# Kernel tuning notes

Hardware: AMD Instinct MI355X
Metric: run time of the kernel (lower is better)

Reference implementation:

```python
import jax, jax.numpy as jnp
import numpy as np

S, B, SC = 2048, 1024, 256 * 16  # shops, bundles, styles*colors


def setup_inputs() -> dict:
    key = jax.random.key(0)
    k1, k2, k3, k4 = jax.random.split(key, 4)
    return {
        "proba": jax.random.normal(k1, (S * B,), dtype=jnp.float32),
        "cur_inven": jax.random.uniform(k2, (S, SC), dtype=jnp.float32),
        "bun_sc": jax.random.uniform(k3, (B, SC), dtype=jnp.float32),
        "avail_bundle": jax.random.uniform(k4, (B,), dtype=jnp.float32),
        "alloc_bundle": jnp.zeros((B,), dtype=jnp.float32),
    }


def reference(proba, cur_inven, bun_sc, avail_bundle, alloc_bundle):
    # proba[i] with i = shop*B + bundle  ->  [S, B]
    p = proba.reshape(S, B)
    # constraint_multiplier: 0.01 if over-availability (p>0) or over-negative-alloc (p<0)
    over_avail = (avail_bundle[None, :] - p < 0.0) & (p > 0.0)
    over_alloc = (alloc_bundle[None, :] + p < 0.0) & (p < 0.0)
    cm = jnp.where(over_avail | over_alloc, jnp.float32(0.01), jnp.float32(1.0))
    # next_inven[s, sc] = cur[s, sc] + sum_b bun_sc[b, sc] * p[s, b] * cm[s, b]
    next_inven = cur_inven + jnp.einsum('sb,bc->sc', p * cm, bun_sc)
    return next_inven.reshape(1, -1)
```

## Files before the change

### kernel.cpp

```cpp
#include <hip/hip_runtime.h>

#define S_DIM  2048
#define B_DIM  1024
#define SC_DIM 4096

#define BM 64
#define BN 128
#define BK 64

typedef __bf16 bf16x8 __attribute__((ext_vector_type(8)));
typedef float  f32x4  __attribute__((ext_vector_type(4)));
typedef unsigned short u16x4 __attribute__((ext_vector_type(4)));
typedef unsigned short u16x8 __attribute__((ext_vector_type(8)));

__device__ __forceinline__ unsigned short f2bf(float f) {
    unsigned int u = __builtin_bit_cast(unsigned int, f);
    return (unsigned short)((u + 0x7FFFu + ((u >> 16) & 1u)) >> 16);
}

__device__ __forceinline__ void gld_lds16(const void* g, void* l) {
    __builtin_amdgcn_global_load_lds(
        (const __attribute__((address_space(1))) unsigned int*)g,
        (__attribute__((address_space(3))) unsigned int*)l, 16, 0, 0);
}

__global__ __launch_bounds__(256)
void prepack_a(const float* __restrict__ proba,
               const float* __restrict__ avail,
               const float* __restrict__ alloc,
               unsigned short* __restrict__ wsA)
{
    int c = blockIdx.x * 256 + threadIdx.x;
    int n = c >> 7;
    int G = c & 127;
    int k = G * 8;

    f32x4 p0 = *(const f32x4*)&proba[(size_t)n * B_DIM + k];
    f32x4 p1 = *(const f32x4*)&proba[(size_t)n * B_DIM + k + 4];
    f32x4 av0 = *(const f32x4*)&avail[k];
    f32x4 av1 = *(const f32x4*)&avail[k + 4];
    f32x4 al0 = *(const f32x4*)&alloc[k];
    f32x4 al1 = *(const f32x4*)&alloc[k + 4];

    u16x8 w;
    #pragma unroll
    for (int i = 0; i < 4; ++i) {
        float pv = p0[i];
        bool oa = (av0[i] - pv < 0.f) && (pv > 0.f);
        bool ob = (al0[i] + pv < 0.f) && (pv < 0.f);
        w[i] = f2bf(pv * ((oa || ob) ? 0.01f : 1.0f));
    }
    #pragma unroll
    for (int i = 0; i < 4; ++i) {
        float pv = p1[i];
        bool oa = (av1[i] - pv < 0.f) && (pv > 0.f);
        bool ob = (al1[i] + pv < 0.f) && (pv < 0.f);
        w[4 + i] = f2bf(pv * ((oa || ob) ? 0.01f : 1.0f));
    }
    int Gs = (G & ~7) | ((G & 7) ^ (n & 7));
    *(u16x8*)&wsA[(size_t)n * B_DIM + Gs * 8] = w;
}

__global__ __launch_bounds__(256)
void prepack_b(const float* __restrict__ bsc,
               unsigned short* __restrict__ wsB)
{
    __shared__ float lds[64][129];
    const int t = threadIdx.x;
    const int bn0 = blockIdx.x * 128;
    const int k0  = blockIdx.y * 64;

    #pragma unroll
    for (int p = 0; p < 8; ++p) {
        int kl = (t >> 5) + p * 8;
        int cl = (t & 31) * 4;
        f32x4 v = *(const f32x4*)&bsc[(size_t)(k0 + kl) * SC_DIM + bn0 + cl];
        lds[kl][cl]     = v[0];
        lds[kl][cl + 1] = v[1];
        lds[kl][cl + 2] = v[2];
        lds[kl][cl + 3] = v[3];
    }
    __syncthreads();

    #pragma unroll
    for (int p = 0; p < 4; ++p) {
        int g = t & 7;
        int n = (t >> 3) + p * 32;
        u16x8 w;
        #pragma unroll
        for (int i = 0; i < 8; ++i)
            w[i] = f2bf(lds[g * 8 + i][n]);
        int gs = g ^ (n & 7);
        *(u16x8*)&wsB[(size_t)(bn0 + n) * B_DIM + k0 + gs * 8] = w;
    }
}

__global__ __launch_bounds__(256, 4)
void gemm_pk(const unsigned short* __restrict__ wsA,
             const unsigned short* __restrict__ wsB,
             const float* __restrict__ cur,
             float* __restrict__ out)
{
    __shared__ __align__(16) unsigned short sA[BM * BK];
    __shared__ __align__(16) unsigned short sB[BN * BK];

    const int tid  = threadIdx.x;
    const int lane = tid & 63;
    const int wid  = tid >> 6;
    const int wm   = wid >> 1;
    const int wn   = wid & 1;
    const int l16  = lane & 15;
    const int lg   = lane >> 4;

    const int bid  = blockIdx.y * gridDim.x + blockIdx.x;
    const int swz  = (bid & 7) * 128 + (bid >> 3);
    const int bm0  = (swz >> 5) * BM;
    const int bn0  = (swz & 31) * BN;

    const int crow = tid >> 3;
    const int cg   = tid & 7;

    f32x4 acc[2][4];
    #pragma unroll
    for (int i = 0; i < 2; ++i)
        #pragma unroll
        for (int j = 0; j < 4; ++j)
            acc[i][j] = {0.f, 0.f, 0.f, 0.f};

    auto stage = [&](int k0) {
        #pragma unroll
        for (int is = 0; is < 2; ++is)
            gld_lds16(wsA + (size_t)(bm0 + is * 32 + crow) * B_DIM + k0 + cg * 8,
                      &sA[(is * 256 + tid) * 8]);
        #pragma unroll
        for (int is = 0; is < 4; ++is)
            gld_lds16(wsB + (size_t)(bn0 + is * 32 + crow) * B_DIM + k0 + cg * 8,
                      &sB[(is * 256 + tid) * 8]);
    };

    auto compute = [&]() {
        #pragma unroll
        for (int kk = 0; kk < 2; ++kk) {
            bf16x8 afr[2], bfr[4];
            #pragma unroll
            for (int mf = 0; mf < 2; ++mf) {
                int r = wm * 32 + mf * 16 + l16;
                afr[mf] = *(const bf16x8*)&sA[r * BK + (((kk * 4 + lg) ^ (r & 7)) * 8)];
            }
            #pragma unroll
            for (int nf = 0; nf < 4; ++nf) {
                int r = wn * 64 + nf * 16 + l16;
                bfr[nf] = *(const bf16x8*)&sB[r * BK + (((kk * 4 + lg) ^ (r & 7)) * 8)];
            }
            __builtin_amdgcn_s_setprio(1);
            #pragma unroll
            for (int mf = 0; mf < 2; ++mf)
                #pragma unroll
                for (int nf = 0; nf < 4; ++nf)
                    acc[mf][nf] = __builtin_amdgcn_mfma_f32_16x16x32_bf16(
                        afr[mf], bfr[nf], acc[mf][nf], 0, 0, 0);
            __builtin_amdgcn_s_setprio(0);
        }
    };

    const int NT = B_DIM / BK;

    for (int t = 0; t < NT - 1; ++t) {
        stage(t * BK);
        __syncthreads();
        compute();
        __syncthreads();
    }

    stage((NT - 1) * BK);
    __syncthreads();

    float cpref[2][4][4];
    #pragma unroll
    for (int mf = 0; mf < 2; ++mf)
        #pragma unroll
        for (int j = 0; j < 4; ++j)
            #pragma unroll
            for (int nf = 0; nf < 4; ++nf) {
                int row = bm0 + wm * 32 + mf * 16 + lg * 4 + j;
                int col = bn0 + wn * 64 + nf * 16 + l16;
                cpref[mf][j][nf] = cur[(size_t)row * SC_DIM + col];
            }

    compute();

    #pragma unroll
    for (int mf = 0; mf < 2; ++mf)
        #pragma unroll
        for (int j = 0; j < 4; ++j)
            #pragma unroll
            for (int nf = 0; nf < 4; ++nf) {
                int row = bm0 + wm * 32 + mf * 16 + lg * 4 + j;
                int col = bn0 + wn * 64 + nf * 16 + l16;
                out[(size_t)row * SC_DIM + col] = cpref[mf][j][nf] + acc[mf][nf][j];
            }
}

#define FBM 128
#define FBN 128
#define LDK 72
__global__ __launch_bounds__(256, 2)
void opt_gemm_fused(const float* __restrict__ proba,
                    const float* __restrict__ cur,
                    const float* __restrict__ bsc,
                    const float* __restrict__ avail,
                    const float* __restrict__ alloc,
                    float* __restrict__ out)
{
    __shared__ __align__(16) unsigned short sA[FBM * LDK];
    __shared__ __align__(16) unsigned short sB[FBN * LDK];
    const int tid = threadIdx.x;
    const int lane = tid & 63;
    const int wid = tid >> 6;
    const int wm = wid >> 1, wn = wid & 1;
    const int bm0 = blockIdx.y * FBM, bn0 = blockIdx.x * FBN;
    const int af4 = tid & 15, ar0 = tid >> 4;
    const int bnn = tid & 127, bkh = tid >> 7;
    const int l16 = lane & 15, lg = lane >> 4;

    f32x4 acc[4][4];
    #pragma unroll
    for (int i = 0; i < 4; ++i)
        #pragma unroll
        for (int j = 0; j < 4; ++j) acc[i][j] = {0.f, 0.f, 0.f, 0.f};

    for (int k0 = 0; k0 < B_DIM; k0 += BK) {
        f32x4 av = *(const f32x4*)&avail[k0 + af4 * 4];
        f32x4 al = *(const f32x4*)&alloc[k0 + af4 * 4];
        #pragma unroll
        for (int pass = 0; pass < 8; ++pass) {
            int r = ar0 + pass * 16;
            f32x4 p = *(const f32x4*)&proba[(size_t)(bm0 + r) * B_DIM + k0 + af4 * 4];
            u16x4 w;
            #pragma unroll
            for (int i = 0; i < 4; ++i) {
                float pv = p[i];
                bool oa = (av[i] - pv < 0.f) && (pv > 0.f);
                bool ob = (al[i] + pv < 0.f) && (pv < 0.f);
                w[i] = f2bf(pv * ((oa || ob) ? 0.01f : 1.0f));
            }
            *(u16x4*)&sA[r * LDK + af4 * 4] = w;
        }
        #pragma unroll
        for (int g = 0; g < 4; ++g) {
            u16x8 w;
            #pragma unroll
            for (int i = 0; i < 8; ++i) {
                int kk = bkh * 32 + g * 8 + i;
                w[i] = f2bf(bsc[(size_t)(k0 + kk) * SC_DIM + bn0 + bnn]);
            }
            *(u16x8*)&sB[bnn * LDK + bkh * 32 + g * 8] = w;
        }
        __syncthreads();
        #pragma unroll
        for (int kk = 0; kk < 2; ++kk) {
            bf16x8 afr[4], bfr[4];
            #pragma unroll
            for (int mf = 0; mf < 4; ++mf)
                afr[mf] = *(const bf16x8*)&sA[(wm * 64 + mf * 16 + l16) * LDK + kk * 32 + lg * 8];
            #pragma unroll
            for (int nf = 0; nf < 4; ++nf)
                bfr[nf] = *(const bf16x8*)&sB[(wn * 64 + nf * 16 + l16) * LDK + kk * 32 + lg * 8];
            #pragma unroll
            for (int mf = 0; mf < 4; ++mf)
                #pragma unroll
                for (int nf = 0; nf < 4; ++nf)
                    acc[mf][nf] = __builtin_amdgcn_mfma_f32_16x16x32_bf16(
                        afr[mf], bfr[nf], acc[mf][nf], 0, 0, 0);
        }
        __syncthreads();
    }
    #pragma unroll
    for (int mf = 0; mf < 4; ++mf)
        #pragma unroll
        for (int j = 0; j < 4; ++j) {
            int row = bm0 + wm * 64 + mf * 16 + lg * 4 + j;
            #pragma unroll
            for (int nf = 0; nf < 4; ++nf) {
                int col = bn0 + wn * 64 + nf * 16 + l16;
                size_t idx = (size_t)row * SC_DIM + col;
                out[idx] = cur[idx] + acc[mf][nf][j];
            }
        }
}

extern "C" void kernel_launch(void* const* d_in, const int* in_sizes, int n_in,
                              void* d_out, int out_size, void* d_ws, size_t ws_size,
                              hipStream_t stream) {
    const float* proba = (const float*)d_in[0];
    const float* cur   = (const float*)d_in[1];
    const float* bsc   = (const float*)d_in[2];
    const float* avail = (const float*)d_in[3];
    const float* alloc = (const float*)d_in[4];
    float* out = (float*)d_out;

    const size_t wsA_bytes = (size_t)S_DIM * B_DIM * 2;
    const size_t wsB_bytes = (size_t)SC_DIM * B_DIM * 2;

    if (ws_size >= wsA_bytes + wsB_bytes) {
        unsigned short* wsA = (unsigned short*)d_ws;
        unsigned short* wsB = (unsigned short*)((char*)d_ws + wsA_bytes);

        prepack_a<<<dim3(S_DIM * B_DIM / 8 / 256), 256, 0, stream>>>(proba, avail, alloc, wsA);
        prepack_b<<<dim3(SC_DIM / 128, B_DIM / 64), 256, 0, stream>>>(bsc, wsB);
        gemm_pk<<<dim3(SC_DIM / BN, S_DIM / BM), 256, 0, stream>>>(wsA, wsB, cur, out);
    } else {
        opt_gemm_fused<<<dim3(SC_DIM / FBN, S_DIM / FBM), 256, 0, stream>>>(
            proba, cur, bsc, avail, alloc, out);
    }
}
```

Measured before the change: 43.57 us.

## Use 512-thread blocks with 8 waves and XCD-aware tile mapping in GEMM

Doubles the GEMM block to 512 threads (8 waves in a 2x4 layout), so each wave computes a 32x32 sub-tile and each thread issues one global-to-LDS copy per operand slice. Block indices are remapped so groups of neighbouring N tiles land on the same XCD, aiming for better L2 reuse. The prefetch of the `cur` epilogue values that overlapped the last compute step is dropped in favour of a simpler loop with `cur` read at store time. More waves per block raise latency hiding but double the LDS-operand reads per MFMA and require heavier barrier synchronisation.

```diff
diff --git a/kernel.cpp b/kernel.cpp
--- a/kernel.cpp
+++ b/kernel.cpp
@@ -95,7 +95,7 @@
     }
 }
 
-__global__ __launch_bounds__(256, 4)
+__global__ __launch_bounds__(512, 8)
 void gemm_pk(const unsigned short* __restrict__ wsA,
              const unsigned short* __restrict__ wsB,
              const float* __restrict__ cur,
@@ -107,97 +107,75 @@
     const int tid  = threadIdx.x;
     const int lane = tid & 63;
     const int wid  = tid >> 6;
-    const int wm   = wid >> 1;
-    const int wn   = wid & 1;
+    const int wm   = wid >> 2;
+    const int wn   = wid & 3;
     const int l16  = lane & 15;
     const int lg   = lane >> 4;
 
-    const int bid  = blockIdx.y * gridDim.x + blockIdx.x;
-    const int swz  = (bid & 7) * 128 + (bid >> 3);
-    const int bm0  = (swz >> 5) * BM;
-    const int bn0  = (swz & 31) * BN;
+    const int bid    = blockIdx.x;
+    const int x      = bid & 7;
+    const int l      = bid >> 3;
+    const int n_tile = x * 4 + (l & 3);
+    const int m_tile = l >> 2;
+    const int bm0    = m_tile * BM;
+    const int bn0    = n_tile * BN;
 
     const int crow = tid >> 3;
     const int cg   = tid & 7;
 
-    f32x4 acc[2][4];
+    f32x4 acc[2][2];
     #pragma unroll
     for (int i = 0; i < 2; ++i)
         #pragma unroll
-        for (int j = 0; j < 4; ++j)
+        for (int j = 0; j < 2; ++j)
             acc[i][j] = {0.f, 0.f, 0.f, 0.f};
 
-    auto stage = [&](int k0) {
-        #pragma unroll
-        for (int is = 0; is < 2; ++is)
-            gld_lds16(wsA + (size_t)(bm0 + is * 32 + crow) * B_DIM + k0 + cg * 8,
-                      &sA[(is * 256 + tid) * 8]);
-        #pragma unroll
-        for (int is = 0; is < 4; ++is)
-            gld_lds16(wsB + (size_t)(bn0 + is * 32 + crow) * B_DIM + k0 + cg * 8,
-                      &sB[(is * 256 + tid) * 8]);
-    };
-
-    auto compute = [&]() {
+    const unsigned short* gA = wsA + (size_t)(bm0 + crow) * B_DIM + cg * 8;
+    const unsigned short* gB0 = wsB + (size_t)(bn0 + crow) * B_DIM + cg * 8;
+    const unsigned short* gB1 = wsB + (size_t)(bn0 + 64 + crow) * B_DIM + cg * 8;
+
+    for (int t = 0; t < B_DIM / BK; ++t) {
+        const int k0 = t * BK;
+        gld_lds16(gA + k0,  &sA[tid * 8]);
+        gld_lds16(gB0 + k0, &sB[tid * 8]);
+        gld_lds16(gB1 + k0, &sB[(512 + tid) * 8]);
+        __syncthreads();
+
         #pragma unroll
         for (int kk = 0; kk < 2; ++kk) {
-            bf16x8 afr[2], bfr[4];
+            bf16x8 afr[2], bfr[2];
             #pragma unroll
             for (int mf = 0; mf < 2; ++mf) {
                 int r = wm * 32 + mf * 16 + l16;
                 afr[mf] = *(const bf16x8*)&sA[r * BK + (((kk * 4 + lg) ^ (r & 7)) * 8)];
             }
             #pragma unroll
-            for (int nf = 0; nf < 4; ++nf) {
-                int r = wn * 64 + nf * 16 + l16;
+            for (int nf = 0; nf < 2; ++nf) {
+                int r = wn * 32 + nf * 16 + l16;
                 bfr[nf] = *(const bf16x8*)&sB[r * BK + (((kk * 4 + lg) ^ (r & 7)) * 8)];
             }
             __builtin_amdgcn_s_setprio(1);
             #pragma unroll
             for (int mf = 0; mf < 2; ++mf)
                 #pragma unroll
-                for (int nf = 0; nf < 4; ++nf)
+                for (int nf = 0; nf < 2; ++nf)
                     acc[mf][nf] = __builtin_amdgcn_mfma_f32_16x16x32_bf16(
                         afr[mf], bfr[nf], acc[mf][nf], 0, 0, 0);
             __builtin_amdgcn_s_setprio(0);
         }
-    };
-
-    const int NT = B_DIM / BK;
-
-    for (int t = 0; t < NT - 1; ++t) {
-        stage(t * BK);
-        __syncthreads();
-        compute();
-        __syncthreads();
-    }
-
-    stage((NT - 1) * BK);
-    __syncthreads();
-
-    float cpref[2][4][4];
+        __syncthreads();
+    }
+
     #pragma unroll
     for (int mf = 0; mf < 2; ++mf)
         #pragma unroll
         for (int j = 0; j < 4; ++j)
             #pragma unroll
-            for (int nf = 0; nf < 4; ++nf) {
+            for (int nf = 0; nf < 2; ++nf) {
                 int row = bm0 + wm * 32 + mf * 16 + lg * 4 + j;
-                int col = bn0 + wn * 64 + nf * 16 + l16;
-                cpref[mf][j][nf] = cur[(size_t)row * SC_DIM + col];
-            }
-
-    compute();
-
-    #pragma unroll
-    for (int mf = 0; mf < 2; ++mf)
-        #pragma unroll
-        for (int j = 0; j < 4; ++j)
-            #pragma unroll
-            for (int nf = 0; nf < 4; ++nf) {
-                int row = bm0 + wm * 32 + mf * 16 + lg * 4 + j;
-                int col = bn0 + wn * 64 + nf * 16 + l16;
-                out[(size_t)row * SC_DIM + col] = cpref[mf][j][nf] + acc[mf][nf][j];
+                int col = bn0 + wn * 32 + nf * 16 + l16;
+                size_t idx = (size_t)row * SC_DIM + col;
+                out[idx] = cur[idx] + acc[mf][nf][j];
             }
 }
 
@@ -308,7 +286,7 @@
 
         prepack_a<<<dim3(S_DIM * B_DIM / 8 / 256), 256, 0, stream>>>(proba, avail, alloc, wsA);
         prepack_b<<<dim3(SC_DIM / 128, B_DIM / 64), 256, 0, stream>>>(bsc, wsB);
-        gemm_pk<<<dim3(SC_DIM / BN, S_DIM / BM), 256, 0, stream>>>(wsA, wsB, cur, out);
+        gemm_pk<<<dim3((S_DIM / BM) * (SC_DIM / BN)), 512, 0, stream>>>(wsA, wsB, cur, out);
     } else {
         opt_gemm_fused<<<dim3(SC_DIM / FBN, S_DIM / FBM), 256, 0, stream>>>(
             proba, cur, bsc, avail, alloc, out);
```

Result: faster. 41.71 us (-4.3%).
